# Performance work log

Measured on AMD Instinct MI355X. Metric: run time of the kernel, lower is better.

Reference implementation:

```python
import jax, jax.numpy as jnp
import numpy as np

# Model hyperparameters (match init_kwargs)
N_HEADS = 16
N_KV_HEADS = 4
HEAD_DIM = 128
ROPE_THETA = 10000.0
WINDOW = 1024  # sliding window (left), right window = 0
SOFTCAP = 50.0
B, T, C = 2, 2048, 2048
G = N_HEADS // N_KV_HEADS


def _sine_table(features, length, max_timescale):
    # min_timescale = 1.0 in the original
    fraction = jnp.arange(0, features, 2, dtype=jnp.float32) / features
    inv_timescale = 1.0 / (max_timescale ** fraction)
    sinusoid = jnp.einsum('i,j->ij', jnp.arange(length), inv_timescale,
                          precision=jax.lax.Precision.HIGHEST)
    sinusoid = jnp.concatenate([sinusoid, sinusoid], axis=-1)  # [T, H]
    return jnp.sin(sinusoid), jnp.cos(sinusoid)


def _rotate_half(x):
    x1, x2 = jnp.split(x, 2, axis=-1)
    return jnp.concatenate([-x2, x1], axis=-1)


def setup_inputs() -> dict:
    key = jax.random.key(0)
    kx, kq, kk, kv, ko = jax.random.split(key, 5)
    x = jax.random.normal(kx, (B, T, C), dtype=jnp.float32)
    init = lambda k, shape: 0.02 * jax.random.normal(k, shape, dtype=jnp.float32)
    q_kernel = init(kq, (C, N_HEADS * HEAD_DIM))
    k_kernel = init(kk, (C, N_KV_HEADS * HEAD_DIM))
    v_kernel = init(kv, (C, N_KV_HEADS * HEAD_DIM))
    out_kernel = init(ko, (N_HEADS * HEAD_DIM, C))
    return {"x": x, "q_kernel": q_kernel, "k_kernel": k_kernel,
            "v_kernel": v_kernel, "out_kernel": out_kernel}


def _attention(x, q_kernel, k_kernel, v_kernel, out_kernel):
    Bs, Ts, Cs = x.shape
    K, H, Gn = N_KV_HEADS, HEAD_DIM, G
    q = jnp.dot(x, q_kernel).reshape(Bs, Ts, K, Gn, H)
    k = jnp.dot(x, k_kernel).reshape(Bs, Ts, K, H)
    v = jnp.dot(x, v_kernel).reshape(Bs, Ts, K, H)

    # RoPE: cos/sin broadcast along the T axis (axis 1), over heads.
    sin, cos = _sine_table(H, Ts, ROPE_THETA)
    qcos = cos[None, :, None, None, :]
    qsin = sin[None, :, None, None, :]
    kcos = cos[None, :, None, :]
    ksin = sin[None, :, None, :]
    q = (q * qcos + _rotate_half(q) * qsin).astype(q.dtype)
    k = (k * kcos + _rotate_half(k) * ksin).astype(k.dtype)

    # Causal + sliding-window mask: key <= query <= key + WINDOW
    pos = jnp.arange(Ts)
    mask = (pos[:, None] >= pos[None, :]) & (pos[:, None] <= pos[None, :] + WINDOW)
    mask = mask[None, None, :, :]  # [1,1,T,S]
    neg = jnp.asarray(-0.7 * jnp.finfo(jnp.float32).max, dtype=jnp.float32)

    scale = jnp.asarray(H ** (-0.5), dtype=q.dtype)
    encoded = []
    for i in range(Gn):  # fixed, small group loop (matches GQA structure)
        qi = q[:, :, :, i] * scale                              # [B,T,K,H]
        logits = jnp.einsum('BTKH,BSKH->BKTS', qi, k)
        logits = jnp.tanh(logits / SOFTCAP) * SOFTCAP           # softcap
        logits = jnp.where(mask, logits, neg)
        probs = jax.nn.softmax(logits.astype(jnp.float32), axis=-1).astype(logits.dtype)
        encoded.append(jnp.einsum('BKTS,BSKH->BTKH', probs, v))
    encoded = jnp.stack(encoded, axis=3)                        # [B,T,K,G,H]
    encoded = encoded.reshape(Bs, Ts, N_HEADS * H)
    return jnp.dot(encoded, out_kernel)


def reference(x, q_kernel, k_kernel, v_kernel, out_kernel):
    return _attention(x, q_kernel, k_kernel, v_kernel, out_kernel)
```

## Files before the change

kernel.cpp:

```cpp
#include <hip/hip_runtime.h>
#include <hip/hip_bf16.h>
#include <math.h>

#define BB 2
#define TT 2048
#define CC 2048
#define NH 16
#define NKV 4
#define HD 128
#define BT (BB*TT)
#define WINDOW 1024
#define SQKV 3072

typedef unsigned short u16;
typedef unsigned int u32;
typedef __attribute__((ext_vector_type(8))) short short8;
typedef __attribute__((ext_vector_type(8))) unsigned short ushort8;
typedef __attribute__((ext_vector_type(4))) unsigned short ushort4v;
typedef __attribute__((ext_vector_type(2))) unsigned int uint2v;
typedef __attribute__((ext_vector_type(4))) float floatx4;
typedef __attribute__((ext_vector_type(16))) float floatx16;

typedef const __attribute__((address_space(1))) u32* gas_ptr;
typedef __attribute__((address_space(3))) u32* las_ptr;

static __device__ __forceinline__ u16 f2bf(float f) {
    unsigned u = __builtin_bit_cast(unsigned, f);
    return (u16)((u + 0x7fffu + ((u >> 16) & 1u)) >> 16);
}
static __device__ __forceinline__ float bf2f(u16 v) {
    unsigned u = ((unsigned)v) << 16;
    return __builtin_bit_cast(float, u);
}

static __device__ __forceinline__ u32 cvt_pk_bf16(float lo, float hi) {
    u32 r;
    asm("v_cvt_pk_bf16_f32 %0, %1, %2" : "=v"(r) : "v"(lo), "v"(hi));
    return r;
}

static __device__ __forceinline__ float softcap_exp(float s) {
    float t = s * 0.02f;
    t = fmaxf(-1.0f, fminf(1.0f, t));
    float t2 = t * t;
    float e = t * fmaf(t2, fmaf(t2, 9.617967f, -24.044917f), 72.134752f);
    return __builtin_amdgcn_exp2f(e);
}

__global__ void cast_bf16_kernel(const float* __restrict__ in, u16* __restrict__ out, int n4) {
    int i = blockIdx.x * blockDim.x + threadIdx.x;
    if (i >= n4) return;
    floatx4 v = *(const floatx4*)(in + (size_t)i * 4);
    ushort4v o;
    o[0] = f2bf(v[0]); o[1] = f2bf(v[1]); o[2] = f2bf(v[2]); o[3] = f2bf(v[3]);
    *(ushort4v*)(out + (size_t)i * 4) = o;
}

__global__ void transpose_cast_f32_kernel(const float* __restrict__ in, u16* __restrict__ out,
                                          int R, int Cc) {
    __shared__ u16 tile[32][33];
    int c0 = blockIdx.x * 32, r0 = blockIdx.y * 32;
    int tx = threadIdx.x, ty = threadIdx.y;
    #pragma unroll
    for (int i = 0; i < 4; i++) {
        int r = r0 + ty + i * 8;
        tile[ty + i * 8][tx] = f2bf(in[(size_t)r * Cc + c0 + tx]);
    }
    __syncthreads();
    #pragma unroll
    for (int i = 0; i < 4; i++) {
        int c = c0 + ty + i * 8;
        out[(size_t)c * R + r0 + tx] = tile[tx][ty + i * 8];
    }
}

__global__ void trig_table_kernel(float* __restrict__ tab) {
    int t = blockIdx.x, j = threadIdx.x;
    float inv = exp2f(-0.20762050593046f * (float)j);
    float s, c;
    sincosf((float)t * inv, &s, &c);
    float* p = tab + (t * 64 + j) * 2;
    p[0] = c; p[1] = s;
}

__global__ void rope_fast_kernel(u16* __restrict__ buf, const float* __restrict__ tab,
                                 int rowStride, float scale) {
    int bt = blockIdx.x;
    int t = bt & (TT - 1);
    int tid = threadIdx.x;
    int h = tid >> 4;
    int j0 = (tid & 15) * 4;
    u16* p = buf + (size_t)bt * rowStride + h * HD + j0;
    ushort4v lo = *(const ushort4v*)(p);
    ushort4v hi = *(const ushort4v*)(p + 64);
    const float* tb = tab + (t * 64 + j0) * 2;
    ushort4v olo, ohi;
    #pragma unroll
    for (int i = 0; i < 4; i++) {
        float c = tb[2 * i], s = tb[2 * i + 1];
        float x1 = bf2f(lo[i]), x2 = bf2f(hi[i]);
        olo[i] = f2bf((x1 * c - x2 * s) * scale);
        ohi[i] = f2bf((x2 * c + x1 * s) * scale);
    }
    *(ushort4v*)(p) = olo;
    *(ushort4v*)(p + 64) = ohi;
}

template <int OMODE>
__global__ __launch_bounds__(256) void gemm128_kernel(const u16* __restrict__ A,
                                                      const u16* __restrict__ Bt,
                                                      void* __restrict__ Cout,
                                                      u16* __restrict__ Vt,
                                                      int M, int N, int K) {
    __shared__ alignas(16) u16 As[128 * 32];
    __shared__ alignas(16) u16 Bs[128 * 32];
    int tid = threadIdx.x;
    int w = tid >> 6, lane = tid & 63, quad = lane >> 4, ln = lane & 15;
    int m0 = blockIdx.y * 128;
    int n0 = blockIdx.x * 128;
    int wm = (w >> 1) * 64;
    int wn = (w & 1) * 64;

    int o0 = (w * 2) * 1024 + lane * 16;
    int row0 = o0 >> 6, kc0 = (o0 & 63) >> 4;
    int o1 = o0 + 1024;
    int row1 = o1 >> 6, kc1 = (o1 & 63) >> 4;
    const u16* gA0 = A  + (size_t)(m0 + row0) * K + kc0 * 8;
    const u16* gA1 = A  + (size_t)(m0 + row1) * K + kc1 * 8;
    const u16* gB0 = Bt + (size_t)(n0 + row0) * K + kc0 * 8;
    const u16* gB1 = Bt + (size_t)(n0 + row1) * K + kc1 * 8;
    u16* lA0 = As + (w * 2) * 512;
    u16* lA1 = As + (w * 2 + 1) * 512;
    u16* lB0 = Bs + (w * 2) * 512;
    u16* lB1 = Bs + (w * 2 + 1) * 512;

    floatx4 acc[4][4] = {};

    for (int k0 = 0; k0 < K; k0 += 32) {
        __syncthreads();
        __builtin_amdgcn_global_load_lds((gas_ptr)(gA0 + k0), (las_ptr)lA0, 16, 0, 0);
        __builtin_amdgcn_global_load_lds((gas_ptr)(gA1 + k0), (las_ptr)lA1, 16, 0, 0);
        __builtin_amdgcn_global_load_lds((gas_ptr)(gB0 + k0), (las_ptr)lB0, 16, 0, 0);
        __builtin_amdgcn_global_load_lds((gas_ptr)(gB1 + k0), (las_ptr)lB1, 16, 0, 0);
        __syncthreads();

        short8 af[4], bf[4];
        #pragma unroll
        for (int mt = 0; mt < 4; mt++)
            af[mt] = *(const short8*)(As + (wm + mt * 16 + ln) * 32 + quad * 8);
        #pragma unroll
        for (int nt = 0; nt < 4; nt++)
            bf[nt] = *(const short8*)(Bs + (wn + nt * 16 + ln) * 32 + quad * 8);
        #pragma unroll
        for (int mt = 0; mt < 4; mt++)
            #pragma unroll
            for (int nt = 0; nt < 4; nt++)
                acc[mt][nt] = __builtin_amdgcn_mfma_f32_16x16x32_bf16(af[mt], bf[nt], acc[mt][nt], 0, 0, 0);
    }

    if (OMODE == 2 && n0 >= 2560) {
        int b = m0 >> 11;
        int tb = (m0 & (TT - 1)) + wm;
        #pragma unroll
        for (int mt = 0; mt < 4; mt++)
          #pragma unroll
          for (int nt = 0; nt < 4; nt++) {
              int c = n0 + wn + nt * 16 + ln - 2560;
              int t0 = tb + mt * 16 + quad * 4;
              ushort4v o;
              #pragma unroll
              for (int r = 0; r < 4; r++) o[r] = f2bf(acc[mt][nt][r]);
              *(ushort4v*)(Vt + (size_t)b * (NKV * HD) * TT + (size_t)c * TT + t0) = o;
          }
    } else {
        #pragma unroll
        for (int mt = 0; mt < 4; mt++)
          #pragma unroll
          for (int nt = 0; nt < 4; nt++)
            #pragma unroll
            for (int r = 0; r < 4; r++) {
                size_t row = m0 + wm + mt * 16 + quad * 4 + r;
                size_t col = n0 + wn + nt * 16 + ln;
                float v = acc[mt][nt][r];
                if (OMODE == 1) ((float*)Cout)[row * N + col] = v;
                else            ((u16*)Cout)[row * N + col] = f2bf(v);
            }
    }
}

__global__ __launch_bounds__(256, 2) void attn_kernel(const u16* __restrict__ QKV,
                                                      const u16* __restrict__ Vt,
                                                      u16* __restrict__ Enc) {
    __shared__ alignas(16) u16 pool[2 * 8192];

    int tid = threadIdx.x;
    int w = tid >> 6, lane = tid & 63, hi = lane >> 5, ln = lane & 31;
    int hi8 = hi * 8;

    int qb = (15 - (int)blockIdx.x) * 128;
    int bh = blockIdx.y;
    int b = bh >> 4, h = bh & 15, kh = h >> 2;
    int qw = qb + w * 32;

    short8 qf[8];
    {
        const u16* qptr = QKV + (size_t)(b * TT + qw + ln) * SQKV + h * HD + hi8;
        #pragma unroll
        for (int ks = 0; ks < 8; ks++) qf[ks] = *(const short8*)(qptr + ks * 16);
    }

    int sig = (ln & 3) + (((ln >> 3) & 1) << 2) + (((ln >> 2) & 1) << 3) + ((ln >> 4) << 4);
    bool isK = (w < 2);
    const u16* dsrc[4];
    int ldst[4];
    #pragma unroll
    for (int i = 0; i < 4; i++) {
        if (isK) {
            int ks = w * 4 + i;
            dsrc[i] = QKV + (size_t)(b * TT + sig) * SQKV + 2048 + kh * HD + ks * 16 + hi8;
            ldst[i] = ks * 512;
        } else {
            int g = (w - 2) * 4 + i;
            dsrc[i] = Vt + (size_t)((b * NKV + kh) * HD + (g >> 1) * 32 + ln) * TT + (g & 1) * 16 + hi8;
            ldst[i] = 4096 + g * 512;
        }
    }
    size_t addmul = isK ? (size_t)SQKV : (size_t)1;

    floatx16 O0 = {}, O1 = {}, O2 = {}, O3 = {};
    float lacc = 0.0f;

    int S_LO = qb - WINDOW; if (S_LO < 0) S_LO = 0;
    int nt = (qb + 128 - S_LO) >> 5;

    auto issue = [&](int t) {
        int s0 = S_LO + t * 32;
        u16* base = pool + (t & 1) * 8192;
        size_t add = (size_t)s0 * addmul;
        #pragma unroll
        for (int i = 0; i < 4; i++)
            __builtin_amdgcn_global_load_lds((gas_ptr)(dsrc[i] + add), (las_ptr)(base + ldst[i]), 16, 0, 0);
    };

    issue(0);
    for (int t = 0; t < nt; ++t) {
        __builtin_amdgcn_sched_barrier(0);
        __builtin_amdgcn_s_barrier();
        __builtin_amdgcn_sched_barrier(0);
        if (t + 1 < nt) {
            issue(t + 1);
            __builtin_amdgcn_sched_barrier(0);
            __builtin_amdgcn_s_waitcnt(0x0F74);
        } else {
            __builtin_amdgcn_s_waitcnt(0x0F70);
        }
        __builtin_amdgcn_sched_barrier(0);
        __builtin_amdgcn_s_barrier();
        __builtin_amdgcn_sched_barrier(0);

        int s0 = S_LO + t * 32;
        if (s0 > qw + 31 || s0 + 31 < qw - WINDOW) continue;

        const u16* Kb = pool + (t & 1) * 8192;
        const u16* Vb = Kb + 4096;

        floatx16 S = {};
        #pragma unroll
        for (int ks = 0; ks < 8; ks++) {
            short8 kf = *(const short8*)(Kb + ks * 512 + lane * 8);
            S = __builtin_amdgcn_mfma_f32_32x32x16_bf16(kf, qf[ks], S, 0, 0, 0);
        }

        bool full = (s0 + 31 <= qw) && (s0 >= qw + 31 - WINDOW);
        if (full) {
            #pragma unroll
            for (int r = 0; r < 16; r++) S[r] = softcap_exp(S[r]);
        } else {
            int tq = qw + ln;
            #pragma unroll
            for (int r = 0; r < 16; r++) {
                int s = s0 + (r & 3) + (((r >> 2) & 1) << 2) + hi8 + ((r >> 3) << 4);
                bool good = (s <= tq) && (s >= tq - WINDOW);
                S[r] = good ? softcap_exp(S[r]) : 0.0f;
            }
        }

        lacc += ((((S[0] + S[1]) + (S[2] + S[3])) + ((S[4] + S[5]) + (S[6] + S[7])))
               + (((S[8] + S[9]) + (S[10] + S[11])) + ((S[12] + S[13]) + (S[14] + S[15]))));

        u32 w0a = cvt_pk_bf16(S[0],  S[1]),  w0b = cvt_pk_bf16(S[2],  S[3]);
        u32 w0c = cvt_pk_bf16(S[4],  S[5]),  w0d = cvt_pk_bf16(S[6],  S[7]);
        u32 w1a = cvt_pk_bf16(S[8],  S[9]),  w1b = cvt_pk_bf16(S[10], S[11]);
        u32 w1c = cvt_pk_bf16(S[12], S[13]), w1d = cvt_pk_bf16(S[14], S[15]);
        typedef __attribute__((ext_vector_type(4))) unsigned int u32x4t;
        u32x4t pw0 = { w0a, w0b, w0c, w0d };
        u32x4t pw1 = { w1a, w1b, w1c, w1d };
        short8 pf0 = __builtin_bit_cast(short8, pw0);
        short8 pf1 = __builtin_bit_cast(short8, pw1);

        #pragma unroll
        for (int dt = 0; dt < 4; dt++) {
            short8 vf0 = *(const short8*)(Vb + (dt * 2 + 0) * 512 + lane * 8);
            short8 vf1 = *(const short8*)(Vb + (dt * 2 + 1) * 512 + lane * 8);
            floatx16* Od = (dt == 0) ? &O0 : (dt == 1) ? &O1 : (dt == 2) ? &O2 : &O3;
            *Od = __builtin_amdgcn_mfma_f32_32x32x16_bf16(vf0, pf0, *Od, 0, 0, 0);
            *Od = __builtin_amdgcn_mfma_f32_32x32x16_bf16(vf1, pf1, *Od, 0, 0, 0);
        }
    }

    __syncthreads();

    lacc += __shfl_xor(lacc, 32);
    float inv = __builtin_amdgcn_rcpf(lacc);
    u16* ep = pool + w * 1024;
    const floatx16* Os[4] = { &O0, &O1, &O2, &O3 };
    #pragma unroll
    for (int dt = 0; dt < 4; dt++) {
        #pragma unroll
        for (int g = 0; g < 4; g++) {
            float a0 = (*Os[dt])[g * 4 + 0] * inv, a1 = (*Os[dt])[g * 4 + 1] * inv;
            float a2 = (*Os[dt])[g * 4 + 2] * inv, a3 = (*Os[dt])[g * 4 + 3] * inv;
            uint2v pk;
            pk[0] = cvt_pk_bf16(a0, a1);
            pk[1] = cvt_pk_bf16(a2, a3);
            *(uint2v*)(ep + ln * 32 + g * 8 + hi * 4) = pk;
        }
        ushort8 r0 = *(const ushort8*)(ep + ln * 32 + hi * 16);
        ushort8 r1 = *(const ushort8*)(ep + ln * 32 + hi * 16 + 8);
        u16* dst = Enc + (size_t)(b * TT + qw + ln) * (NH * HD) + h * HD + dt * 32 + hi * 16;
        *(ushort8*)dst = r0;
        *(ushort8*)(dst + 8) = r1;
    }
}

extern "C" void kernel_launch(void* const* d_in, const int* in_sizes, int n_in,
                              void* d_out, int out_size, void* d_ws, size_t ws_size,
                              hipStream_t stream) {
    const float* x  = (const float*)d_in[0];
    const float* wq = (const float*)d_in[1];
    const float* wk = (const float*)d_in[2];
    const float* wv = (const float*)d_in[3];
    const float* wo = (const float*)d_in[4];
    float* out = (float*)d_out;

    char* ws = (char*)d_ws;
    size_t off = 0;
    auto alloc = [&](size_t bytes) -> void* {
        void* p = ws + off;
        off += (bytes + 255) & ~(size_t)255;
        return p;
    };
    u16* xb    = (u16*)alloc((size_t)BT * CC * 2);
    u16* wqkvT = (u16*)alloc((size_t)SQKV * CC * 2);
    u16* woT   = (u16*)alloc((size_t)CC * CC * 2);
    u16* QKVb  = (u16*)alloc((size_t)BT * SQKV * 2);
    u16* VtT   = (u16*)alloc((size_t)BT * NKV * HD * 2);
    u16* Enc   = (u16*)alloc((size_t)BT * NH * HD * 2);
    float* trig = (float*)alloc((size_t)TT * 64 * 2 * 4);

    trig_table_kernel<<<TT, 64, 0, stream>>>(trig);

    cast_bf16_kernel<<<(BT * CC / 4 + 255) / 256, 256, 0, stream>>>(x, xb, BT * CC / 4);
    dim3 tb(32, 8);
    transpose_cast_f32_kernel<<<dim3(CC / 32, CC / 32), tb, 0, stream>>>(wq, wqkvT, CC, CC);
    transpose_cast_f32_kernel<<<dim3(NKV * HD / 32, CC / 32), tb, 0, stream>>>(wk, wqkvT + (size_t)2048 * CC, CC, NKV * HD);
    transpose_cast_f32_kernel<<<dim3(NKV * HD / 32, CC / 32), tb, 0, stream>>>(wv, wqkvT + (size_t)2560 * CC, CC, NKV * HD);
    transpose_cast_f32_kernel<<<dim3(CC / 32, CC / 32), tb, 0, stream>>>(wo, woT, CC, CC);

    gemm128_kernel<2><<<dim3(SQKV / 128, BT / 128), 256, 0, stream>>>(xb, wqkvT, QKVb, VtT, BT, SQKV, CC);

    rope_fast_kernel<<<BT, NH * 16, 0, stream>>>(QKVb, trig, SQKV, 0.08838834764831845f);
    rope_fast_kernel<<<BT, NKV * 16, 0, stream>>>(QKVb + 2048, trig, SQKV, 1.0f);

    attn_kernel<<<dim3(16, 32), 256, 0, stream>>>(QKVb, VtT, Enc);

    gemm128_kernel<1><<<dim3(CC / 128, BT / 128), 256, 0, stream>>>(Enc, woT, out, nullptr, BT, CC, CC);
}
```

Before: 315.4 us.

## Merge prep kernels, fuse rope with trig table, and relayout GEMM LDS tiles

The five cast and transpose kernels become one prep launch that picks its work by block index. The two RoPE launches and the trig-table kernel become one rope kernel that computes sin/cos into shared memory per row. The GEMM global-to-LDS loads are reorganized so each 16-row fragment is stored contiguously, making fragment reads simple lane*8 offsets. This cuts launch overhead and the trig table's global traffic, at the cost of recomputing sincos for every token row and possibly different LDS bank behaviour.

After: 345.4 us. 9.5% more time.

```diff
diff --git a/kernel.cpp b/kernel.cpp
--- a/kernel.cpp
+++ b/kernel.cpp
@@ -47,20 +47,34 @@
     return __builtin_amdgcn_exp2f(e);
 }
 
-__global__ void cast_bf16_kernel(const float* __restrict__ in, u16* __restrict__ out, int n4) {
-    int i = blockIdx.x * blockDim.x + threadIdx.x;
-    if (i >= n4) return;
-    floatx4 v = *(const floatx4*)(in + (size_t)i * 4);
-    ushort4v o;
-    o[0] = f2bf(v[0]); o[1] = f2bf(v[1]); o[2] = f2bf(v[2]); o[3] = f2bf(v[3]);
-    *(ushort4v*)(out + (size_t)i * 4) = o;
-}
-
-__global__ void transpose_cast_f32_kernel(const float* __restrict__ in, u16* __restrict__ out,
-                                          int R, int Cc) {
+__global__ __launch_bounds__(256) void prep_kernel(const float* __restrict__ x,
+                                                   const float* __restrict__ wq,
+                                                   const float* __restrict__ wk,
+                                                   const float* __restrict__ wv,
+                                                   const float* __restrict__ wo,
+                                                   u16* __restrict__ xb,
+                                                   u16* __restrict__ wqkvT,
+                                                   u16* __restrict__ woT) {
     __shared__ u16 tile[32][33];
-    int c0 = blockIdx.x * 32, r0 = blockIdx.y * 32;
-    int tx = threadIdx.x, ty = threadIdx.y;
+    int bid = blockIdx.x;
+    int tid = threadIdx.x;
+    if (bid < 8192) {
+        int i = bid * 256 + tid;
+        floatx4 v = *(const floatx4*)(x + (size_t)i * 4);
+        ushort4v o;
+        o[0] = f2bf(v[0]); o[1] = f2bf(v[1]); o[2] = f2bf(v[2]); o[3] = f2bf(v[3]);
+        *(ushort4v*)(xb + (size_t)i * 4) = o;
+        return;
+    }
+    bid -= 8192;
+    const float* in; u16* out; int Cc, bx, by;
+    if (bid < 4096)      { in = wq; out = wqkvT;                    Cc = 2048; bx = bid & 63; by = bid >> 6; }
+    else if (bid < 5120) { bid -= 4096; in = wk; out = wqkvT + (size_t)2048 * CC; Cc = 512; bx = bid & 15; by = bid >> 4; }
+    else if (bid < 6144) { bid -= 5120; in = wv; out = wqkvT + (size_t)2560 * CC; Cc = 512; bx = bid & 15; by = bid >> 4; }
+    else                 { bid -= 6144; in = wo; out = woT;         Cc = 2048; bx = bid & 63; by = bid >> 6; }
+    const int R = 2048;
+    int c0 = bx * 32, r0 = by * 32;
+    int tx = tid & 31, ty = tid >> 5;
     #pragma unroll
     for (int i = 0; i < 4; i++) {
         int r = r0 + ty + i * 8;
@@ -74,30 +88,30 @@
     }
 }
 
-__global__ void trig_table_kernel(float* __restrict__ tab) {
-    int t = blockIdx.x, j = threadIdx.x;
-    float inv = exp2f(-0.20762050593046f * (float)j);
-    float s, c;
-    sincosf((float)t * inv, &s, &c);
-    float* p = tab + (t * 64 + j) * 2;
-    p[0] = c; p[1] = s;
-}
-
-__global__ void rope_fast_kernel(u16* __restrict__ buf, const float* __restrict__ tab,
-                                 int rowStride, float scale) {
+__global__ __launch_bounds__(320) void rope_kernel(u16* __restrict__ buf) {
+    __shared__ float tab[128];
     int bt = blockIdx.x;
     int t = bt & (TT - 1);
     int tid = threadIdx.x;
-    int h = tid >> 4;
-    int j0 = (tid & 15) * 4;
-    u16* p = buf + (size_t)bt * rowStride + h * HD + j0;
+    if (tid < 64) {
+        float inv = exp2f(-0.20762050593046f * (float)tid);
+        float s, c;
+        sincosf((float)t * inv, &s, &c);
+        tab[tid * 2] = c; tab[tid * 2 + 1] = s;
+    }
+    __syncthreads();
+    bool isQ = tid < 256;
+    int loc = isQ ? tid : tid - 256;
+    int h = loc >> 4;
+    int j0 = (loc & 15) * 4;
+    float scale = isQ ? 0.08838834764831845f : 1.0f;
+    u16* p = buf + (size_t)bt * SQKV + (isQ ? 0 : 2048) + h * HD + j0;
     ushort4v lo = *(const ushort4v*)(p);
     ushort4v hi = *(const ushort4v*)(p + 64);
-    const float* tb = tab + (t * 64 + j0) * 2;
     ushort4v olo, ohi;
     #pragma unroll
     for (int i = 0; i < 4; i++) {
-        float c = tb[2 * i], s = tb[2 * i + 1];
+        float c = tab[(j0 + i) * 2], s = tab[(j0 + i) * 2 + 1];
         float x1 = bf2f(lo[i]), x2 = bf2f(hi[i]);
         olo[i] = f2bf((x1 * c - x2 * s) * scale);
         ohi[i] = f2bf((x2 * c + x1 * s) * scale);
@@ -112,8 +126,8 @@
                                                       void* __restrict__ Cout,
                                                       u16* __restrict__ Vt,
                                                       int M, int N, int K) {
-    __shared__ alignas(16) u16 As[128 * 32];
-    __shared__ alignas(16) u16 Bs[128 * 32];
+    __shared__ alignas(16) u16 As[4096];
+    __shared__ alignas(16) u16 Bs[4096];
     int tid = threadIdx.x;
     int w = tid >> 6, lane = tid & 63, quad = lane >> 4, ln = lane & 15;
     int m0 = blockIdx.y * 128;
@@ -121,36 +135,33 @@
     int wm = (w >> 1) * 64;
     int wn = (w & 1) * 64;
 
-    int o0 = (w * 2) * 1024 + lane * 16;
-    int row0 = o0 >> 6, kc0 = (o0 & 63) >> 4;
-    int o1 = o0 + 1024;
-    int row1 = o1 >> 6, kc1 = (o1 & 63) >> 4;
-    const u16* gA0 = A  + (size_t)(m0 + row0) * K + kc0 * 8;
-    const u16* gA1 = A  + (size_t)(m0 + row1) * K + kc1 * 8;
-    const u16* gB0 = Bt + (size_t)(n0 + row0) * K + kc0 * 8;
-    const u16* gB1 = Bt + (size_t)(n0 + row1) * K + kc1 * 8;
-    u16* lA0 = As + (w * 2) * 512;
-    u16* lA1 = As + (w * 2 + 1) * 512;
-    u16* lB0 = Bs + (w * 2) * 512;
-    u16* lB1 = Bs + (w * 2 + 1) * 512;
+    const u16* gsrc[4];
+    u16* ldstp[4];
+    #pragma unroll
+    for (int j = 0; j < 4; j++) {
+        int g = j * 4 + w;
+        int f = g & 7;
+        const u16* base = (g < 8) ? (A + (size_t)m0 * K) : (Bt + (size_t)n0 * K);
+        gsrc[j] = base + (size_t)(f * 16 + ln) * K + quad * 8;
+        ldstp[j] = (g < 8 ? As : Bs) + f * 512;
+    }
 
     floatx4 acc[4][4] = {};
 
     for (int k0 = 0; k0 < K; k0 += 32) {
         __syncthreads();
-        __builtin_amdgcn_global_load_lds((gas_ptr)(gA0 + k0), (las_ptr)lA0, 16, 0, 0);
-        __builtin_amdgcn_global_load_lds((gas_ptr)(gA1 + k0), (las_ptr)lA1, 16, 0, 0);
-        __builtin_amdgcn_global_load_lds((gas_ptr)(gB0 + k0), (las_ptr)lB0, 16, 0, 0);
-        __builtin_amdgcn_global_load_lds((gas_ptr)(gB1 + k0), (las_ptr)lB1, 16, 0, 0);
+        #pragma unroll
+        for (int j = 0; j < 4; j++)
+            __builtin_amdgcn_global_load_lds((gas_ptr)(gsrc[j] + k0), (las_ptr)ldstp[j], 16, 0, 0);
         __syncthreads();
 
         short8 af[4], bf[4];
         #pragma unroll
         for (int mt = 0; mt < 4; mt++)
-            af[mt] = *(const short8*)(As + (wm + mt * 16 + ln) * 32 + quad * 8);
+            af[mt] = *(const short8*)(As + ((w >> 1) * 4 + mt) * 512 + lane * 8);
         #pragma unroll
         for (int nt = 0; nt < 4; nt++)
-            bf[nt] = *(const short8*)(Bs + (wn + nt * 16 + ln) * 32 + quad * 8);
+            bf[nt] = *(const short8*)(Bs + ((w & 1) * 4 + nt) * 512 + lane * 8);
         #pragma unroll
         for (int mt = 0; mt < 4; mt++)
             #pragma unroll
@@ -356,21 +367,12 @@
     u16* QKVb  = (u16*)alloc((size_t)BT * SQKV * 2);
     u16* VtT   = (u16*)alloc((size_t)BT * NKV * HD * 2);
     u16* Enc   = (u16*)alloc((size_t)BT * NH * HD * 2);
-    float* trig = (float*)alloc((size_t)TT * 64 * 2 * 4);
-
-    trig_table_kernel<<<TT, 64, 0, stream>>>(trig);
-
-    cast_bf16_kernel<<<(BT * CC / 4 + 255) / 256, 256, 0, stream>>>(x, xb, BT * CC / 4);
-    dim3 tb(32, 8);
-    transpose_cast_f32_kernel<<<dim3(CC / 32, CC / 32), tb, 0, stream>>>(wq, wqkvT, CC, CC);
-    transpose_cast_f32_kernel<<<dim3(NKV * HD / 32, CC / 32), tb, 0, stream>>>(wk, wqkvT + (size_t)2048 * CC, CC, NKV * HD);
-    transpose_cast_f32_kernel<<<dim3(NKV * HD / 32, CC / 32), tb, 0, stream>>>(wv, wqkvT + (size_t)2560 * CC, CC, NKV * HD);
-    transpose_cast_f32_kernel<<<dim3(CC / 32, CC / 32), tb, 0, stream>>>(wo, woT, CC, CC);
+
+    prep_kernel<<<18432, 256, 0, stream>>>(x, wq, wk, wv, wo, xb, wqkvT, woT);
 
     gemm128_kernel<2><<<dim3(SQKV / 128, BT / 128), 256, 0, stream>>>(xb, wqkvT, QKVb, VtT, BT, SQKV, CC);
 
-    rope_fast_kernel<<<BT, NH * 16, 0, stream>>>(QKVb, trig, SQKV, 0.08838834764831845f);
-    rope_fast_kernel<<<BT, NKV * 16, 0, stream>>>(QKVb + 2048, trig, SQKV, 1.0f);
+    rope_kernel<<<BT, 320, 0, stream>>>(QKVb);
 
     attn_kernel<<<dim3(16, 32), 256, 0, stream>>>(QKVb, VtT, Enc);
 
```
